# Optimization experiments

Measured on AMD Instinct MI355X. Metric: run time of the kernel, lower is better.

The kernel has to match this reference:

```python
import jax, jax.numpy as jnp
import numpy as np

MODEL_DIM = 2048
Q_HEADS = 32
KV_HEADS = 8
HEAD_DIM = MODEL_DIM // Q_HEADS  # 64
ROPE_BASE = 10000.0


def apply_rope(x, pos):
    # x: [B, S, H, D], interleaved-pair RoPE (torchtune-style)
    half = x.shape[-1] // 2
    inv_freq = 1.0 / (ROPE_BASE ** (jnp.arange(half, dtype=jnp.float32) * 2.0 / x.shape[-1]))
    ang = pos.astype(jnp.float32)[:, None] * inv_freq[None, :]        # [S, half]
    cos = jnp.cos(ang)[None, :, None, :]                              # [1,S,1,half]
    sin = jnp.sin(ang)[None, :, None, :]
    x1 = x[..., 0::2]
    x2 = x[..., 1::2]
    o1 = x1 * cos - x2 * sin
    o2 = x2 * cos + x1 * sin
    return jnp.stack([o1, o2], axis=-1).reshape(x.shape)


def setup_inputs() -> dict:
    key = jax.random.key(0)
    ks = jax.random.split(key, 5)
    B, S, D = 2, 2048, MODEL_DIM
    sd = 1.0 / np.sqrt(D)
    x = jax.random.normal(ks[0], (B, S, D), dtype=jnp.float32)
    wq = jax.random.normal(ks[1], (Q_HEADS * HEAD_DIM, D), dtype=jnp.float32) * sd
    wk = jax.random.normal(ks[2], (KV_HEADS * HEAD_DIM, D), dtype=jnp.float32) * sd
    wv = jax.random.normal(ks[3], (KV_HEADS * HEAD_DIM, D), dtype=jnp.float32) * sd
    wo = jax.random.normal(ks[4], (D, D), dtype=jnp.float32) * sd
    attention_mask = jnp.ones((B, S), dtype=bool)
    return {"x": x, "attention_mask": attention_mask, "wq": wq, "wk": wk, "wv": wv, "wo": wo}


def reference(x, attention_mask, wq, wk, wv, wo):
    B, S, D = x.shape
    rep = Q_HEADS // KV_HEADS
    q = (x @ wq.T).reshape(B, S, Q_HEADS, HEAD_DIM)
    k = (x @ wk.T).reshape(B, S, KV_HEADS, HEAD_DIM)
    v = (x @ wv.T).reshape(B, S, KV_HEADS, HEAD_DIM)
    # GQA repeat_interleave along head axis
    k = jnp.repeat(k, rep, axis=2)
    v = jnp.repeat(v, rep, axis=2)
    pos = jnp.arange(S)
    q = apply_rope(q, pos)
    k = apply_rope(k, pos)
    # scores [B, H, Sq, Sk]
    score = jnp.einsum('bqhd,bkhd->bhqk', q, k) / np.sqrt(HEAD_DIM)
    neg_inf = jnp.finfo(score.dtype).min
    causal = jnp.tril(jnp.ones((S, S), dtype=bool))
    score = jnp.where(causal[None, None, :, :], score, neg_inf)
    score = jnp.where(attention_mask[:, None, None, :], score, neg_inf)
    attn = jax.nn.softmax(score, axis=-1)
    out = jnp.einsum('bhqk,bkhd->bqhd', attn, v).reshape(B, S, D)
    return out @ wo.T
```

## Files before the change

kernel.cpp:

```cpp
#include <hip/hip_runtime.h>
#include <hip/hip_bf16.h>

#define S_LEN 2048
#define BATCH 2
#define DMODEL 2048
#define HQ 32
#define HKV 8
#define HD 64
#define NQ 2560
#define KDIM 2048

typedef __attribute__((ext_vector_type(8))) short bf16x8;
typedef __attribute__((ext_vector_type(4))) float f32x4;

#if __has_builtin(__builtin_amdgcn_exp2f)
#define EXP2(x) __builtin_amdgcn_exp2f(x)
#else
#define EXP2(x) exp2f(x)
#endif

template<int N> struct ic { static constexpr int value = N; };

static __device__ inline ushort f2bf(float f) {
    union { float f; unsigned u; } v; v.f = f;
    unsigned r = v.u + 0x7fff + ((v.u >> 16) & 1);
    return (ushort)(r >> 16);
}
static __device__ inline float bf2f(ushort h) {
    union { unsigned u; float f; } v; v.u = ((unsigned)h) << 16; return v.f;
}
static __device__ inline unsigned pack2(float lo, float hi) {
    return (unsigned)f2bf(lo) | ((unsigned)f2bf(hi) << 16);
}
static __device__ __forceinline__ unsigned pkbf(float lo, float hi) {
    union { float f; unsigned u; } a, b; a.f = lo; b.f = hi;
    return __builtin_amdgcn_perm(b.u + 0x8000u, a.u + 0x8000u, 0x07060302u);
}

static __device__ __forceinline__ void gload16(const ushort* g, ushort* l) {
    __builtin_amdgcn_global_load_lds(
        (const __attribute__((address_space(1))) unsigned int*)(g),
        (__attribute__((address_space(3))) unsigned int*)(l), 16, 0, 0);
}

#define BARRIER() asm volatile("s_barrier" ::: "memory")
#define WAITVM(N) asm volatile("s_waitcnt vmcnt(" #N ")" ::: "memory")

__global__ __launch_bounds__(256) void convert_kernel(const float* __restrict__ x,
                                                      const float* __restrict__ wq,
                                                      const float* __restrict__ wk,
                                                      const float* __restrict__ wv,
                                                      const float* __restrict__ wo,
                                                      ushort* __restrict__ xb,
                                                      ushort* __restrict__ wqkvb,
                                                      ushort* __restrict__ wob)
{
    size_t e = ((size_t)blockIdx.x * 256 + threadIdx.x) * 8;
    const float* src; ushort* dst;
    if (e < 8388608ul)       { src = x  + e;              dst = xb + e; }
    else if (e < 12582912ul) { src = wq + (e - 8388608);  dst = wqkvb + (e - 8388608); }
    else if (e < 13631488ul) { src = wk + (e - 12582912); dst = wqkvb + 4194304 + (e - 12582912); }
    else if (e < 14680064ul) { src = wv + (e - 13631488); dst = wqkvb + 5242880 + (e - 13631488); }
    else                     { src = wo + (e - 14680064); dst = wob + (e - 14680064); }
    float4 a = *(const float4*)src;
    float4 b = *(const float4*)(src + 4);
    uint4 p; p.x = pack2(a.x, a.y); p.y = pack2(a.z, a.w);
             p.z = pack2(b.x, b.y); p.w = pack2(b.z, b.w);
    *(uint4*)dst = p;
}

template<int BNF, int EPI>
__global__ __launch_bounds__(512, 2) void gemm256(const ushort* __restrict__ A,
                                                  const ushort* __restrict__ Bw,
                                                  ushort* __restrict__ qkv,
                                                  ushort* __restrict__ vT,
                                                  float* __restrict__ Cf)
{
    constexpr int BN = BNF * 64;
    constexpr int KT = KDIM / 64;
    __shared__ ushort As[2][256 * 64];
    __shared__ ushort Bs[2][BN * 64];
    const int t    = threadIdx.x;
    const int w    = t >> 6, lane = t & 63;
    const int quad = lane >> 4, l15 = lane & 15;
    const int l8   = lane >> 3;
    const int scw  = ((lane & 7) ^ (l8 & 7)) * 8;
    const int wm   = (w >> 2) * 128;
    const int wn   = (w & 3) * (BNF * 16);

    const int bid = blockIdx.x;
    const int sb  = (bid & 7) * 32 + (bid >> 3);
    const int mb  = (sb >> 4) * 256;
    const int nb  = (sb & 15) * BN;

    f32x4 acc[8][BNF] = {};
    bf16x8 a[4][2], b[BNF][2];

    auto SAH = [&](int buf, int half, int kb) {
        #pragma unroll
        for (int L = 0; L < 2; L++) {
            int r0 = half * 128 + (w * 2 + L) * 8;
            gload16(A + (size_t)(mb + r0 + l8) * KDIM + kb + scw, &As[buf][r0 * 64]);
        }
    };
    auto SB = [&](int buf, int kb) {
        #pragma unroll
        for (int L = 0; L < BNF; L++) {
            int r0 = (w * BNF + L) * 8;
            gload16(Bw + (size_t)(nb + r0 + l8) * KDIM + kb + scw, &Bs[buf][r0 * 64]);
        }
    };
    auto LA = [&](int buf, int hm) {
        #pragma unroll
        for (int i = 0; i < 4; i++) {
            int r = wm + hm * 64 + i * 16 + l15;
            int rs = r * 64, sw = r & 7;
            #pragma unroll
            for (int kc = 0; kc < 2; kc++)
                a[i][kc] = *(const bf16x8*)&As[buf][rs + (((kc << 2) | quad) ^ sw) * 8];
        }
    };
    auto LB = [&](int buf) {
        #pragma unroll
        for (int j = 0; j < BNF; j++) {
            int r = wn + j * 16 + l15;
            int rs = r * 64, sw = r & 7;
            #pragma unroll
            for (int kc = 0; kc < 2; kc++)
                b[j][kc] = *(const bf16x8*)&Bs[buf][rs + (((kc << 2) | quad) ^ sw) * 8];
        }
    };
    auto MM = [&](auto HM) {
        constexpr int hm = decltype(HM)::value;
        __builtin_amdgcn_s_setprio(1);
        #pragma unroll
        for (int i = 0; i < 4; i++)
            #pragma unroll
            for (int j = 0; j < BNF; j++) {
                f32x4 d = acc[hm * 4 + i][j];
                d = __builtin_amdgcn_mfma_f32_16x16x32_bf16(a[i][0], b[j][0], d, 0, 0, 0);
                d = __builtin_amdgcn_mfma_f32_16x16x32_bf16(a[i][1], b[j][1], d, 0, 0, 0);
                acc[hm * 4 + i][j] = d;
            }
        __builtin_amdgcn_s_setprio(0);
    };

    SAH(0, 0, 0); SAH(0, 1, 0); SB(0, 0);
    SAH(1, 0, 64); SB(1, 64);
    if constexpr (BNF == 3) WAITVM(5); else WAITVM(4);
    BARRIER();

    #pragma unroll 1
    for (int tt = 0; tt < KT - 2; tt++) {
        const int buf = tt & 1, o = buf ^ 1;
        LA(buf, 0); LB(buf);
        SAH(o, 1, (tt + 1) * 64);
        BARRIER();
        MM(ic<0>{});
        if constexpr (BNF == 3) WAITVM(7); else WAITVM(6);
        BARRIER();
        LA(buf, 1);
        SAH(buf, 0, (tt + 2) * 64); SB(buf, (tt + 2) * 64);
        BARRIER();
        MM(ic<1>{});
        if constexpr (BNF == 3) WAITVM(7); else WAITVM(6);
        BARRIER();
    }
    LA(0, 0); LB(0);
    SAH(1, 1, (KT - 1) * 64);
    BARRIER();
    MM(ic<0>{});
    if constexpr (BNF == 3) WAITVM(7); else WAITVM(6);
    BARRIER();
    LA(0, 1);
    BARRIER();
    MM(ic<1>{});
    WAITVM(2);
    BARRIER();
    LA(1, 0); LB(1);
    BARRIER();
    MM(ic<0>{});
    WAITVM(0);
    BARRIER();
    LA(1, 1);
    BARRIER();
    MM(ic<1>{});

    #pragma unroll
    for (int i = 0; i < 8; i++) {
        int m0 = mb + wm + (i >> 2) * 64 + (i & 3) * 16 + quad * 4;
        #pragma unroll
        for (int j = 0; j < BNF; j++) {
            int n0 = nb + wn + j * 16;
            if (EPI == 0) {
                if (n0 >= 2560) {
                    ushort4 pk;
                    pk.x = f2bf(acc[i][j][0]); pk.y = f2bf(acc[i][j][1]);
                    pk.z = f2bf(acc[i][j][2]); pk.w = f2bf(acc[i][j][3]);
                    *(ushort4*)&vT[(size_t)(n0 + l15 - 2560) * 4096 + m0] = pk;
                } else {
                    #pragma unroll
                    for (int r = 0; r < 4; r++)
                        qkv[(size_t)(m0 + r) * NQ + n0 + l15] = f2bf(acc[i][j][r]);
                }
            } else {
                #pragma unroll
                for (int r = 0; r < 4; r++)
                    Cf[(size_t)(m0 + r) * DMODEL + n0 + l15] = acc[i][j][r];
            }
        }
    }
}

__global__ __launch_bounds__(256) void rope_kernel(ushort* __restrict__ qkv)
{
    const int PAIRS = BATCH * S_LEN * (HQ + HKV) * (HD / 2);
    int tid = blockIdx.x * 256 + threadIdx.x;
    if (tid >= PAIRS) return;
    int token = tid / ((HQ + HKV) * 32);
    int r     = tid - token * ((HQ + HKV) * 32);
    int hh    = r >> 5;
    int i     = r & 31;
    int base  = (hh < HQ) ? hh * 64 : DMODEL + (hh - HQ) * 64;
    size_t addr = (size_t)token * NQ + base + 2 * i;
    int s = token & (S_LEN - 1);
    float freq = exp2f(-0.41524101186092f * (float)i);
    float ang  = (float)s * freq;
    float sn, cs;
    sincosf(ang, &sn, &cs);
    float x1 = bf2f(qkv[addr]);
    float x2 = bf2f(qkv[addr + 1]);
    qkv[addr]     = f2bf(x1 * cs - x2 * sn);
    qkv[addr + 1] = f2bf(x2 * cs + x1 * sn);
}

__global__ __launch_bounds__(256) void attn_kernel(const ushort* __restrict__ qkv,
                                                   const ushort* __restrict__ vT,
                                                   ushort* __restrict__ attnb)
{
    __shared__ ushort Ks[2][64 * 64];
    __shared__ ushort VT[2][64 * 64];
    __shared__ ushort PT[4][32 * 72];
    const int t    = threadIdx.x;
    const int w    = t >> 6, lane = t & 63;
    const int quad = lane >> 4, l15 = lane & 15;
    const int bid  = blockIdx.x;
    const int qx   = 15 - (bid >> 6);
    const int h    = bid & 31;
    const int b    = (bid >> 5) & 1;
    const int qb   = qx * 128;
    const int kvh  = h >> 2;
    const ushort* base = qkv + (size_t)b * S_LEN * NQ;
    const ushort* vTb  = vT + (size_t)kvh * HD * 4096 + b * S_LEN;

    const float SC = 0.18033688011112042f;
    bf16x8 aq[2][2];
    #pragma unroll
    for (int h2 = 0; h2 < 2; h2++) {
        const ushort* qp = base + (size_t)(qb + w * 32 + h2 * 16 + l15) * NQ + h * HD + quad * 8;
        #pragma unroll
        for (int hf = 0; hf < 2; hf++) {
            bf16x8 v = *(const bf16x8*)(qp + hf * 32);
            #pragma unroll
            for (int j = 0; j < 8; j++) v[j] = (short)f2bf(bf2f((ushort)v[j]) * SC);
            aq[h2][hf] = v;
        }
    }

    f32x4 o[2][4] = {};
    float lsum[2] = {};
    const int qw    = qb + w * 32;
    const int strow = lane >> 3;
    const int stlc  = (lane & 7) ^ strow;
    ushort* ptw = &PT[w][0];
    const int niter = (qb + 128) / 64;

    #pragma unroll
    for (int c = 0; c < 2; c++) {
        int key = w * 16 + c * 8 + strow;
        gload16(base + (size_t)key * NQ + DMODEL + kvh * HD + stlc * 8,
                &Ks[0][(w * 16 + c * 8) * 64]);
        gload16(vTb + (size_t)key * 4096 + stlc * 8,
                &VT[0][(w * 16 + c * 8) * 64]);
    }

    for (int i = 0; i < niter; i++) {
        const int kb  = i * 64;
        const int cur = i & 1;
        __syncthreads();
        if (i + 1 < niter) {
            int kb2 = kb + 64;
            #pragma unroll
            for (int c = 0; c < 2; c++) {
                int key = w * 16 + c * 8 + strow;
                gload16(base + (size_t)(kb2 + key) * NQ + DMODEL + kvh * HD + stlc * 8,
                        &Ks[1 - cur][(w * 16 + c * 8) * 64]);
                gload16(vTb + (size_t)key * 4096 + kb2 + stlc * 8,
                        &VT[1 - cur][(w * 16 + c * 8) * 64]);
            }
        }
        if (kb <= qw + 31) {
            const bool full = (kb + 63) <= qw;
            const ushort* ks = &Ks[cur][0];
            const ushort* vs = &VT[cur][0];
            f32x4 s[2][4];
            #pragma unroll
            for (int kt = 0; kt < 4; kt++) {
                int key = kt * 16 + l15;
                int sw  = l15 & 7;
                bf16x8 k0 = *(const bf16x8*)&ks[key * 64 + (quad ^ sw) * 8];
                bf16x8 k1 = *(const bf16x8*)&ks[key * 64 + (((quad + 4) & 7) ^ sw) * 8];
                #pragma unroll
                for (int h2 = 0; h2 < 2; h2++) {
                    f32x4 z = {};
                    z = __builtin_amdgcn_mfma_f32_16x16x32_bf16(k0, aq[h2][0], z, 0, 0, 0);
                    z = __builtin_amdgcn_mfma_f32_16x16x32_bf16(k1, aq[h2][1], z, 0, 0, 0);
                    s[h2][kt] = z;
                }
            }
            #pragma unroll
            for (int h2 = 0; h2 < 2; h2++) {
                int rq    = h2 * 16 + l15;
                int wbase = rq * 72 + (quad & 1) * 4;
                #pragma unroll
                for (int kt = 0; kt < 4; kt++) {
                    float p0 = EXP2(s[h2][kt][0]);
                    float p1 = EXP2(s[h2][kt][1]);
                    float p2 = EXP2(s[h2][kt][2]);
                    float p3 = EXP2(s[h2][kt][3]);
                    if (!full) {
                        int key0 = kb + kt * 16 + quad * 4;
                        int q    = qb + w * 32 + rq;
                        p0 = (key0 + 0 <= q) ? p0 : 0.f;
                        p1 = (key0 + 1 <= q) ? p1 : 0.f;
                        p2 = (key0 + 2 <= q) ? p2 : 0.f;
                        p3 = (key0 + 3 <= q) ? p3 : 0.f;
                    }
                    lsum[h2] += (p0 + p1) + (p2 + p3);
                    int pc = kt * 2 + (quad >> 1);
                    uint2 pk;
                    pk.x = pkbf(p0, p1);
                    pk.y = pkbf(p2, p3);
                    *(uint2*)&ptw[wbase + pc * 8] = pk;
                }
            }
            bf16x8 pf[2][2];
            #pragma unroll
            for (int h2 = 0; h2 < 2; h2++) {
                int rq = h2 * 16 + l15;
                #pragma unroll
                for (int kc = 0; kc < 2; kc++)
                    pf[h2][kc] = *(const bf16x8*)&ptw[rq * 72 + (kc * 4 + quad) * 8];
            }
            #pragma unroll
            for (int tt = 0; tt < 4; tt++) {
                int dr = tt * 16 + l15;
                int sw = l15 & 7;
                bf16x8 vf0 = *(const bf16x8*)&vs[dr * 64 + (quad ^ sw) * 8];
                bf16x8 vf1 = *(const bf16x8*)&vs[dr * 64 + (((quad + 4) & 7) ^ sw) * 8];
                #pragma unroll
                for (int h2 = 0; h2 < 2; h2++) {
                    f32x4 oo = o[h2][tt];
                    oo = __builtin_amdgcn_mfma_f32_16x16x32_bf16(vf0, pf[h2][0], oo, 0, 0, 0);
                    oo = __builtin_amdgcn_mfma_f32_16x16x32_bf16(vf1, pf[h2][1], oo, 0, 0, 0);
                    o[h2][tt] = oo;
                }
            }
        }
    }
    #pragma unroll
    for (int h2 = 0; h2 < 2; h2++) {
        float l = lsum[h2];
        l += __shfl_xor(l, 16, 64);
        l += __shfl_xor(l, 32, 64);
        float inv = 1.0f / l;
        ushort* ob = attnb + (size_t)(b * S_LEN + qb + w * 32 + h2 * 16 + l15) * DMODEL
                   + h * HD + quad * 4;
        #pragma unroll
        for (int tt = 0; tt < 4; tt++) {
            uint2 st;
            st.x = pkbf(o[h2][tt][0] * inv, o[h2][tt][1] * inv);
            st.y = pkbf(o[h2][tt][2] * inv, o[h2][tt][3] * inv);
            *(uint2*)&ob[tt * 16] = st;
        }
    }
}

extern "C" void kernel_launch(void* const* d_in, const int* in_sizes, int n_in,
                              void* d_out, int out_size, void* d_ws, size_t ws_size,
                              hipStream_t stream)
{
    const float* x  = (const float*)d_in[0];
    const float* wq = (const float*)d_in[2];
    const float* wk = (const float*)d_in[3];
    const float* wv = (const float*)d_in[4];
    const float* wo = (const float*)d_in[5];
    float* out = (float*)d_out;

    char* ws = (char*)d_ws;
    ushort* qkv    = (ushort*)(ws);
    ushort* vT     = (ushort*)(ws + 20971520);
    ushort* xb     = (ushort*)(ws + 25165824);
    ushort* attn_b = xb;
    ushort* wqkvb  = (ushort*)(ws + 41943040);
    ushort* wob    = (ushort*)(ws + 54525952);

    convert_kernel<<<9216, 256, 0, stream>>>(x, wq, wk, wv, wo, xb, wqkvb, wob);

    gemm256<3, 0><<<256, 512, 0, stream>>>(xb, wqkvb, qkv, vT, nullptr);

    int pairs = BATCH * S_LEN * (HQ + HKV) * (HD / 2);
    rope_kernel<<<(pairs + 255) / 256, 256, 0, stream>>>(qkv);

    attn_kernel<<<1024, 256, 0, stream>>>(qkv, vT, attn_b);

    gemm256<2, 1><<<256, 512, 0, stream>>>(attn_b, wob, nullptr, nullptr, out);
}
```

Before: 273.9 us.

## Keep softmax probabilities in registers by permuting the V-transpose key layout

The attention kernel no longer writes the P tile to shared memory and reads it back as MFMA operands. Instead it packs the probabilities directly into registers with v_cvt_pk_bf16_f32. To make that register layout line up with the PV MFMA's k-dimension, the QKV GEMM epilogue now stores vT with a permuted key index within each 64-key block. This removes an LDS round trip and its bank traffic per iteration, but couples the GEMM epilogue layout to the attention kernel's fragment ordering, and the conversion switches from the manual rounding to the hardware convert instruction.

```diff
diff --git a/kernel.cpp b/kernel.cpp
--- a/kernel.cpp
+++ b/kernel.cpp
@@ -35,6 +35,11 @@
 static __device__ __forceinline__ unsigned pkbf(float lo, float hi) {
     union { float f; unsigned u; } a, b; a.f = lo; b.f = hi;
     return __builtin_amdgcn_perm(b.u + 0x8000u, a.u + 0x8000u, 0x07060302u);
+}
+static __device__ __forceinline__ unsigned cvtpk(float lo, float hi) {
+    unsigned r;
+    asm("v_cvt_pk_bf16_f32 %0, %1, %2" : "=v"(r) : "v"(lo), "v"(hi));
+    return r;
 }
 
 static __device__ __forceinline__ void gload16(const ushort* g, ushort* l) {
@@ -194,10 +199,12 @@
             int n0 = nb + wn + j * 16;
             if (EPI == 0) {
                 if (n0 >= 2560) {
+                    int m0p = (m0 & ~63) | (((m0 >> 5) & 1) << 5)
+                            | (((m0 >> 2) & 3) << 3) | (((m0 >> 4) & 1) << 2);
                     ushort4 pk;
                     pk.x = f2bf(acc[i][j][0]); pk.y = f2bf(acc[i][j][1]);
                     pk.z = f2bf(acc[i][j][2]); pk.w = f2bf(acc[i][j][3]);
-                    *(ushort4*)&vT[(size_t)(n0 + l15 - 2560) * 4096 + m0] = pk;
+                    *(ushort4*)&vT[(size_t)(n0 + l15 - 2560) * 4096 + m0p] = pk;
                 } else {
                     #pragma unroll
                     for (int r = 0; r < 4; r++)
@@ -240,7 +247,6 @@
 {
     __shared__ ushort Ks[2][64 * 64];
     __shared__ ushort VT[2][64 * 64];
-    __shared__ ushort PT[4][32 * 72];
     const int t    = threadIdx.x;
     const int w    = t >> 6, lane = t & 63;
     const int quad = lane >> 4, l15 = lane & 15;
@@ -272,7 +278,6 @@
     const int qw    = qb + w * 32;
     const int strow = lane >> 3;
     const int stlc  = (lane & 7) ^ strow;
-    ushort* ptw = &PT[w][0];
     const int niter = (qb + 128) / 64;
 
     #pragma unroll
@@ -318,10 +323,10 @@
                     s[h2][kt] = z;
                 }
             }
+            bf16x8 pf[2][2];
             #pragma unroll
             for (int h2 = 0; h2 < 2; h2++) {
-                int rq    = h2 * 16 + l15;
-                int wbase = rq * 72 + (quad & 1) * 4;
+                union { unsigned u[8]; bf16x8 v[2]; } pw;
                 #pragma unroll
                 for (int kt = 0; kt < 4; kt++) {
                     float p0 = EXP2(s[h2][kt][0]);
@@ -330,27 +335,18 @@
                     float p3 = EXP2(s[h2][kt][3]);
                     if (!full) {
                         int key0 = kb + kt * 16 + quad * 4;
-                        int q    = qb + w * 32 + rq;
+                        int q    = qb + w * 32 + h2 * 16 + l15;
                         p0 = (key0 + 0 <= q) ? p0 : 0.f;
                         p1 = (key0 + 1 <= q) ? p1 : 0.f;
                         p2 = (key0 + 2 <= q) ? p2 : 0.f;
                         p3 = (key0 + 3 <= q) ? p3 : 0.f;
                     }
                     lsum[h2] += (p0 + p1) + (p2 + p3);
-                    int pc = kt * 2 + (quad >> 1);
-                    uint2 pk;
-                    pk.x = pkbf(p0, p1);
-                    pk.y = pkbf(p2, p3);
-                    *(uint2*)&ptw[wbase + pc * 8] = pk;
+                    pw.u[kt * 2 + 0] = cvtpk(p0, p1);
+                    pw.u[kt * 2 + 1] = cvtpk(p2, p3);
                 }
-            }
-            bf16x8 pf[2][2];
-            #pragma unroll
-            for (int h2 = 0; h2 < 2; h2++) {
-                int rq = h2 * 16 + l15;
-                #pragma unroll
-                for (int kc = 0; kc < 2; kc++)
-                    pf[h2][kc] = *(const bf16x8*)&ptw[rq * 72 + (kc * 4 + quad) * 8];
+                pf[h2][0] = pw.v[0];
+                pf[h2][1] = pw.v[1];
             }
             #pragma unroll
             for (int tt = 0; tt < 4; tt++) {
```

Result: faster. 268.4 us (-2.0%).
